# Kernel optimization log

Measured on AMD Instinct MI355X. Metric: run time of the kernel, lower is better.

Reference implementation:

```python
import jax, jax.numpy as jnp
import numpy as np

B, S, D, H, E, K = 4, 1024, 1024, 4096, 8, 2
CAPACITY_FACTOR = 2.0
T = B * S
CAP = int(T * CAPACITY_FACTOR * K / E)  # 2048


def setup_inputs() -> dict:
    key = jax.random.key(0)
    ks = jax.random.split(key, 6)
    std = 0.02
    return {
        "x": jax.random.normal(ks[0], (B, S, D), dtype=jnp.float32),
        "router_w": jax.random.normal(ks[1], (E, D), dtype=jnp.float32) * std,
        "w1": jax.random.normal(ks[2], (E, D, H), dtype=jnp.float32) * std,
        "b1": jnp.zeros((E, H), dtype=jnp.float32),
        "w2": jax.random.normal(ks[3], (E, H, D), dtype=jnp.float32) * std,
        "b2": jnp.zeros((E, D), dtype=jnp.float32),
    }


def reference(x, router_w, w1, b1, w2, b2):
    # Router (eval mode: no logit noise, no dropout)
    logits = jnp.einsum("bsd,ed->bse", x, router_w)            # [B,S,E]
    probs = jax.nn.softmax(logits, axis=-1)
    topk_p, topk_i = jax.lax.top_k(probs, K)                   # [B,S,K]
    gates = topk_p / jnp.sum(topk_p, axis=-1, keepdims=True)

    xt = x.reshape(T, D)                                        # tokens
    eidx = topk_i.reshape(T * K)                                # expert per slot
    g = gates.reshape(T * K)
    tok = jnp.arange(T * K) // K                                # token id per slot

    # position of each slot within its expert (first-come-first-served capacity)
    oh = jax.nn.one_hot(eidx, E, dtype=jnp.int32)               # [T*K, E]
    pos = jnp.sum((jnp.cumsum(oh, axis=0) - 1) * oh, axis=1)    # [T*K]
    keep = pos < CAP
    pos_c = jnp.where(keep, pos, CAP)                           # overflow -> padding row

    # dispatch: gather tokens into per-expert buffers [E, CAP, D]
    buf = jnp.zeros((E, CAP + 1, D), x.dtype).at[eidx, pos_c].set(xt[tok])
    inp = buf[:, :CAP]

    # per-expert FFN (exact-erf GELU matches torch nn.GELU default)
    h = jax.nn.gelu(jnp.einsum("ecd,edh->ech", inp, w1) + b1[:, None, :],
                    approximate=False)
    out_e = jnp.einsum("ech,eho->eco", h, w2) + b2[:, None, :]  # [E,CAP,D]

    # combine: gather back to slots, weight by gates, sum over k per token
    gathered = out_e[eidx, jnp.minimum(pos_c, CAP - 1)]         # [T*K, D]
    wslot = g * keep.astype(x.dtype)
    out = (gathered * wslot[:, None]).reshape(T, K, D).sum(axis=1).reshape(B, S, D)

    # load-balancing loss
    router_prob_per_expert = probs.mean(axis=(0, 1))            # [E]
    expert_usage = oh.sum(axis=0).astype(x.dtype) / (T * K)
    lb_loss = jnp.sum(router_prob_per_expert * expert_usage) * E
    return out, lb_loss
```

## Files before the change

kernel.cpp:

```cpp
#include <hip/hip_runtime.h>
#include <cstdint>
#include <cstddef>

#define TDIM 4096
#define DDIM 1024
#define HDIM 4096
#define EDIM 8
#define CAPD 2048
#define NSLOT 8192
#define NROUTERBLK 1024

typedef _Float16 f16;
typedef _Float16 f16x2 __attribute__((ext_vector_type(2)));
typedef _Float16 f16x4 __attribute__((ext_vector_type(4)));
typedef _Float16 f16x8 __attribute__((ext_vector_type(8)));
typedef float f32x4 __attribute__((ext_vector_type(4)));

__device__ __forceinline__ void gload16(const void* g, void* l) {
  __builtin_amdgcn_global_load_lds(
      (const __attribute__((address_space(1))) unsigned int*)g,
      (__attribute__((address_space(3))) unsigned int*)l, 16, 0, 0);
}

__device__ __forceinline__ float gelu_fast(float x) {
  float y = 1.5957691216057308f * (x + 0.044715f * x * x * x);
  y = fminf(y, 60.f);
  float e = __expf(y);
  return x * e * __builtin_amdgcn_rcpf(e + 1.f);
}

__global__ __launch_bounds__(256)
void transpose2_cvt(const float* __restrict__ w1, f16* __restrict__ w1t,
                    const float* __restrict__ w2, f16* __restrict__ w2t) {
  __shared__ float tile[128][65];
  const int z = blockIdx.z;
  const int id = blockIdx.y * 64 + blockIdx.x;
  const float* src; f16* dst; int R, C, rt, ct, e;
  if (z < EDIM) {
    e = z; src = w1; dst = w1t; R = DDIM; C = HDIM;
    ct = id & 63; rt = id >> 6;
  } else {
    e = z - EDIM; src = w2; dst = w2t; R = HDIM; C = DDIM;
    ct = id & 15; rt = id >> 4;
  }
  const int tid = threadIdx.x;
  const int r0 = rt * 128, c0 = ct * 64;
  const float* s = src + (size_t)e * R * C;
  f16* d = dst + (size_t)e * R * C;
  #pragma unroll
  for (int it = 0; it < 8; ++it) {
    const int idx = it * 256 + tid;
    const int row = idx >> 4, colq = (idx & 15) * 4;
    float4 v = *(const float4*)(s + (size_t)(r0 + row) * C + c0 + colq);
    tile[row][colq] = v.x; tile[row][colq + 1] = v.y;
    tile[row][colq + 2] = v.z; tile[row][colq + 3] = v.w;
  }
  __syncthreads();
  #pragma unroll
  for (int it = 0; it < 4; ++it) {
    const int idx = it * 256 + tid;
    const int c = idx >> 4, rw = (idx & 15) * 8;
    f16x8 o;
    #pragma unroll
    for (int j = 0; j < 8; ++j) o[j] = (f16)tile[rw + j][c];
    *(f16x8*)(d + (size_t)(c0 + c) * R + r0 + rw) = o;
  }
}

__global__ void router_k(const float* __restrict__ x, const float* __restrict__ rw,
                         int* __restrict__ eidx, float* __restrict__ gates,
                         float* __restrict__ bps) {
  __shared__ float lrw[EDIM * DDIM];
  __shared__ float wps[4][EDIM];
  const int tid = threadIdx.x, lane = tid & 63, wv = tid >> 6;
  for (int i = tid; i < EDIM * DDIM; i += 256) lrw[i] = rw[i];
  __syncthreads();
  const int t = blockIdx.x * 4 + wv;
  float acc[EDIM];
  #pragma unroll
  for (int e = 0; e < EDIM; ++e) acc[e] = 0.f;
  const float* xr = x + (size_t)t * DDIM;
  #pragma unroll
  for (int j = 0; j < DDIM / 64; ++j) {
    float xv = xr[j * 64 + lane];
    #pragma unroll
    for (int e = 0; e < EDIM; ++e) acc[e] += xv * lrw[e * DDIM + j * 64 + lane];
  }
  #pragma unroll
  for (int off = 32; off >= 1; off >>= 1) {
    #pragma unroll
    for (int e = 0; e < EDIM; ++e) acc[e] += __shfl_xor(acc[e], off);
  }
  float mx = acc[0];
  #pragma unroll
  for (int e = 1; e < EDIM; ++e) mx = fmaxf(mx, acc[e]);
  float p[EDIM], s = 0.f;
  #pragma unroll
  for (int e = 0; e < EDIM; ++e) { p[e] = expf(acc[e] - mx); s += p[e]; }
  float inv = 1.f / s;
  #pragma unroll
  for (int e = 0; e < EDIM; ++e) p[e] *= inv;
  int i1 = 0; float p1 = p[0];
  #pragma unroll
  for (int e = 1; e < EDIM; ++e) if (p[e] > p1) { p1 = p[e]; i1 = e; }
  int i2 = (i1 == 0) ? 1 : 0; float p2 = p[i2];
  #pragma unroll
  for (int e = 0; e < EDIM; ++e) if (e != i1 && p[e] > p2) { p2 = p[e]; i2 = e; }
  float gs = 1.f / (p1 + p2);
  if (lane == 0) {
    eidx[2 * t] = i1; eidx[2 * t + 1] = i2;
    gates[2 * t] = p1 * gs; gates[2 * t + 1] = p2 * gs;
    #pragma unroll
    for (int e = 0; e < EDIM; ++e) wps[wv][e] = p[e];
  }
  __syncthreads();
  if (tid < EDIM)
    bps[blockIdx.x * EDIM + tid] = wps[0][tid] + wps[1][tid] + wps[2][tid] + wps[3][tid];
}

__global__ void count_k(const int* __restrict__ eidx, int* __restrict__ cc) {
  __shared__ int h[EDIM];
  const int tid = threadIdx.x;
  if (tid < EDIM) h[tid] = 0;
  __syncthreads();
  atomicAdd(&h[eidx[blockIdx.x * 256 + tid]], 1);
  __syncthreads();
  if (tid < EDIM) cc[blockIdx.x * EDIM + tid] = h[tid];
}

__global__ void scan_k(const int* __restrict__ cc, const float* __restrict__ bps,
                       int* __restrict__ cb, int* __restrict__ counts,
                       int* __restrict__ rowsNeeded, float* __restrict__ lb_out) {
  __shared__ float red[32][EDIM];
  __shared__ int cnt_s[EDIM];
  const int tid = threadIdx.x;
  const int e = tid & 7, g = tid >> 3;
  float s = 0.f;
  for (int j = 0; j < 32; ++j) s += bps[(g + 32 * j) * EDIM + e];
  red[g][e] = s;
  __syncthreads();
  for (int st = 16; st >= 1; st >>= 1) {
    if (g < st) red[g][e] += red[g + st][e];
    __syncthreads();
  }
  if (tid < EDIM) {
    int base = 0;
    for (int c = 0; c < 32; ++c) { cb[c * EDIM + tid] = base; base += cc[c * EDIM + tid]; }
    counts[tid] = base;
    rowsNeeded[tid] = base < CAPD ? base : CAPD;
    cnt_s[tid] = base;
  }
  __syncthreads();
  if (tid == 0) {
    float lb = 0.f;
    for (int ee = 0; ee < EDIM; ++ee)
      lb += (red[0][ee] / (float)TDIM) * ((float)cnt_s[ee] / (float)NSLOT);
    lb_out[0] = lb * (float)EDIM;
  }
}

__global__ void pos_k(const int* __restrict__ eidx, const float* __restrict__ gates,
                      const int* __restrict__ cb, int* __restrict__ posa,
                      float* __restrict__ wslot) {
  __shared__ int wcnt[4][EDIM];
  const int tid = threadIdx.x, lane = tid & 63, wv = tid >> 6;
  const int slot = blockIdx.x * 256 + tid;
  const int e = eidx[slot];
  const unsigned long long below = (1ull << lane) - 1ull;
  int wavepos = 0;
  #pragma unroll
  for (int ee = 0; ee < EDIM; ++ee) {
    unsigned long long m = __ballot(e == ee);
    if (lane == 0) wcnt[wv][ee] = __popcll(m);
    if (e == ee) wavepos = __popcll(m & below);
  }
  __syncthreads();
  int off = 0;
  for (int w = 0; w < wv; ++w) off += wcnt[w][e];
  const int pos = cb[blockIdx.x * EDIM + e] + off + wavepos;
  posa[slot] = pos;
  wslot[slot] = (pos < CAPD) ? gates[slot] : 0.f;
}

__global__ void scatter2_k(const float* __restrict__ x, const int* __restrict__ eidx,
                           const int* __restrict__ posa, f16* __restrict__ buf) {
  const int t = blockIdx.x, lane = threadIdx.x;
  const int s0 = 2 * t, s1 = 2 * t + 1;
  const int p0 = posa[s0], p1 = posa[s1];
  const int e0 = eidx[s0], e1 = eidx[s1];
  const float4* src = (const float4*)(x + (size_t)t * DDIM);
  f16x4* d0 = (f16x4*)(buf + ((size_t)e0 * CAPD + p0) * DDIM);
  f16x4* d1 = (f16x4*)(buf + ((size_t)e1 * CAPD + p1) * DDIM);
  const bool w0 = p0 < CAPD, w1 = p1 < CAPD;
  #pragma unroll
  for (int j = 0; j < DDIM / 4 / 64; ++j) {
    float4 v = src[j * 64 + lane];
    f16x4 o; o.x = (f16)v.x; o.y = (f16)v.y; o.z = (f16)v.z; o.w = (f16)v.w;
    if (w0) d0[j * 64 + lane] = o;
    if (w1) d1[j * 64 + lane] = o;
  }
}

#define STAGE(hh, g) do { \
    const f16* s_ = sP[hh] + (g) * 64; \
    char* d_ = smem + (hh) * 8192 + wv * 1024; \
    gload16(s_, d_); \
    gload16(s_ + (size_t)32 * LD, d_ + 4096); \
  } while (0)

template<int KLEN, int LD, int N, int GELU, int NTH, int NKS, int NMT>
__global__ __launch_bounds__(256, 4)
void gemm128s(const f16* __restrict__ A, const f16* __restrict__ Bt,
              const float* __restrict__ bias, f16* __restrict__ C, size_t pstride,
              const int* __restrict__ rowsNeeded) {
  constexpr int NTT = KLEN / 64;
  __shared__ __align__(128) char smem[32768];
  const int wg = blockIdx.x;
  const int e = wg & 7;
  const int r = wg >> 3;
  const int ntl = r % NTH;
  const int ks = (r / NTH) % NKS;
  const int mt = (r / (NTH * NKS)) % NMT;
  const int nth = r / (NTH * NKS * NMT);
  const int nt = nth * NTH + ntl;
  if (mt * 128 >= rowsNeeded[e]) return;
  const int tid = threadIdx.x, lane = tid & 63, wv = tid >> 6;
  const int wr = wv >> 1, wc = wv & 1;
  const int ro = lane & 15, q4 = (lane >> 4) * 4;
  const int ko0b = (lane >> 4) * 16;
  const f16* aBase = A + ((size_t)e * CAPD + (size_t)mt * 128) * LD + (size_t)ks * KLEN;
  const f16* bBase = Bt + ((size_t)e * N + (size_t)nt * 128) * LD + (size_t)ks * KLEN;
  const int row0 = tid >> 3;
  const int sw0 = ((tid & 7) ^ (row0 & 7)) * 8;

  const f16* sP[4];
  sP[0] = aBase + (size_t)row0 * LD + sw0;
  sP[1] = sP[0] + (size_t)64 * LD;
  sP[2] = bBase + (size_t)row0 * LD + sw0;
  sP[3] = sP[2] + (size_t)64 * LD;

  int aoffs[4][2], boffs[4][2];
  #pragma unroll
  for (int m = 0; m < 4; ++m)
    #pragma unroll
    for (int k = 0; k < 2; ++k) {
      const int rh = wr * 64 + m * 16 + ro;
      aoffs[m][k] = rh * 128 + ((k * 64 + ko0b) ^ ((rh & 7) << 4));
      const int rb = wc * 64 + m * 16 + ro;
      boffs[m][k] = 16384 + rb * 128 + ((k * 64 + ko0b) ^ ((rb & 7) << 4));
    }

  f32x4 acc[4][4];
  #pragma unroll
  for (int m = 0; m < 4; ++m)
    #pragma unroll
    for (int n = 0; n < 4; ++n) acc[m][n] = (f32x4){0.f, 0.f, 0.f, 0.f};

  #pragma unroll 1
  for (int t = 0; t < NTT; ++t) {
    STAGE(0, t); STAGE(1, t); STAGE(2, t); STAGE(3, t);
    __syncthreads();
    f16x8 af[4][2], bf[4][2];
    #pragma unroll
    for (int m = 0; m < 4; ++m)
      #pragma unroll
      for (int k = 0; k < 2; ++k) {
        af[m][k] = *(const f16x8*)(smem + aoffs[m][k]);
        bf[m][k] = *(const f16x8*)(smem + boffs[m][k]);
      }
    #pragma unroll
    for (int k = 0; k < 2; ++k)
      #pragma unroll
      for (int m = 0; m < 4; ++m)
        #pragma unroll
        for (int n = 0; n < 4; ++n)
          acc[m][n] = __builtin_amdgcn_mfma_f32_16x16x32_f16(af[m][k], bf[n][k], acc[m][n], 0, 0, 0);
    __syncthreads();
  }

  float bv[4];
  #pragma unroll
  for (int n = 0; n < 4; ++n)
    bv[n] = (ks == 0) ? bias[e * N + nt * 128 + wc * 64 + n * 16 + ro] : 0.f;
  f16* Ct = (f16*)(smem + wv * 8192);
  #pragma unroll
  for (int m = 0; m < 4; ++m)
    #pragma unroll
    for (int n = 0; n < 4; ++n)
      #pragma unroll
      for (int i = 0; i < 4; ++i) {
        const int row = m * 16 + q4 + i;
        float v = acc[m][n][i] + bv[n];
        if (GELU) v = gelu_fast(v);
        *(f16*)((char*)Ct + row * 128 + (((n * 16 + ro) * 2) ^ (((row >> 2) & 3) << 5))) = (f16)v;
      }
  asm volatile("s_waitcnt lgkmcnt(0)" ::: "memory");
  __builtin_amdgcn_sched_barrier(0);
  f16* Cp = C + (size_t)ks * pstride;
  const size_t crow0 = (size_t)e * CAPD + mt * 128 + wr * 64;
  const int ccol0 = nt * 128 + wc * 64;
  #pragma unroll
  for (int j = 0; j < 8; ++j) {
    const int idx = j * 64 + lane;
    const int rr = idx >> 3, c2 = (idx & 7) * 16;
    f16x8 v = *(const f16x8*)((const char*)Ct + rr * 128 + (c2 ^ (((rr >> 2) & 3) << 5)));
    *(f16x8*)(Cp + (crow0 + rr) * N + ccol0 + (idx & 7) * 8) = v;
  }
}

__global__ void combine_k(const f16* __restrict__ pA, const f16* __restrict__ pB,
                          const int* __restrict__ eidx, const int* __restrict__ posa,
                          const float* __restrict__ wslot, float* __restrict__ out) {
  const int t = blockIdx.x, tid = threadIdx.x;
  const int s0 = 2 * t, s1 = 2 * t + 1;
  const int e0 = eidx[s0], e1 = eidx[s1];
  int p0 = posa[s0]; p0 = p0 < CAPD - 1 ? p0 : CAPD - 1;
  int p1 = posa[s1]; p1 = p1 < CAPD - 1 ? p1 : CAPD - 1;
  const float g0 = wslot[s0], g1 = wslot[s1];
  const size_t o0 = ((size_t)e0 * CAPD + p0) * DDIM;
  const size_t o1 = ((size_t)e1 * CAPD + p1) * DDIM;
  const f16x2* r0a = (const f16x2*)(pA + o0);
  const f16x2* r0b = (const f16x2*)(pB + o0);
  const f16x2* r1a = (const f16x2*)(pA + o1);
  const f16x2* r1b = (const f16x2*)(pB + o1);
  float2* o = (float2*)(out + (size_t)t * DDIM);
  #pragma unroll
  for (int j = tid; j < DDIM / 2; j += 256) {
    f16x2 a0 = r0a[j], a1 = r0b[j], b0 = r1a[j], b1 = r1b[j];
    o[j] = make_float2(
        g0 * ((float)a0.x + (float)a1.x) + g1 * ((float)b0.x + (float)b1.x),
        g0 * ((float)a0.y + (float)a1.y) + g1 * ((float)b0.y + (float)b1.y));
  }
}

extern "C" void kernel_launch(void* const* d_in, const int* in_sizes, int n_in,
                              void* d_out, int out_size, void* d_ws, size_t ws_size,
                              hipStream_t stream) {
  (void)in_sizes; (void)n_in; (void)out_size; (void)ws_size;
  const float* x  = (const float*)d_in[0];
  const float* rw = (const float*)d_in[1];
  const float* w1 = (const float*)d_in[2];
  const float* b1 = (const float*)d_in[3];
  const float* w2 = (const float*)d_in[4];
  const float* b2 = (const float*)d_in[5];
  float* out = (float*)d_out;

  char* ws = (char*)d_ws;
  size_t off = 0;
  auto alloc = [&](size_t b) { void* p = ws + off; off += (b + 255) & ~(size_t)255; return p; };
  f16* w1t   = (f16*)alloc((size_t)EDIM * DDIM * HDIM * 2);
  f16* w2t   = (f16*)alloc((size_t)EDIM * DDIM * HDIM * 2);
  f16* buf   = (f16*)alloc((size_t)EDIM * CAPD * DDIM * 2);
  f16* hbuf  = (f16*)alloc((size_t)EDIM * CAPD * HDIM * 2);
  const size_t PSTRIDE = (size_t)EDIM * CAPD * DDIM;
  f16* outeA = (f16*)alloc(PSTRIDE * 2);
  f16* outeB = (f16*)alloc(PSTRIDE * 2);
  int*   eidx   = (int*)alloc(NSLOT * 4);
  int*   posa   = (int*)alloc(NSLOT * 4);
  float* gatesA = (float*)alloc(NSLOT * 4);
  float* wslotA = (float*)alloc(NSLOT * 4);
  int*   cc     = (int*)alloc(32 * EDIM * 4);
  int*   cb     = (int*)alloc(32 * EDIM * 4);
  int*   counts = (int*)alloc(EDIM * 4);
  int*   rowsN  = (int*)alloc(EDIM * 4);
  float* bps    = (float*)alloc(NROUTERBLK * EDIM * 4);
  (void)outeB;

  transpose2_cvt<<<dim3(64, 8, 2 * EDIM), 256, 0, stream>>>(w1, w1t, w2, w2t);

  router_k<<<NROUTERBLK, 256, 0, stream>>>(x, rw, eidx, gatesA, bps);
  count_k<<<32, 256, 0, stream>>>(eidx, cc);
  scan_k<<<1, 256, 0, stream>>>(cc, bps, cb, counts, rowsN, out + (size_t)TDIM * DDIM);
  pos_k<<<32, 256, 0, stream>>>(eidx, gatesA, cb, posa, wslotA);
  scatter2_k<<<TDIM, 64, 0, stream>>>(x, eidx, posa, buf);

  gemm128s<DDIM, DDIM, HDIM, 1, 16, 1, 16><<<4096, 256, 0, stream>>>(
      buf, w1t, b1, hbuf, 0, rowsN);

  gemm128s<HDIM / 2, HDIM, DDIM, 0, 8, 2, 16><<<2048, 256, 0, stream>>>(
      hbuf, w2t, b2, outeA, PSTRIDE, rowsN);

  combine_k<<<TDIM, 256, 0, stream>>>(outeA, outeA + PSTRIDE, eidx, posa, wslotA, out);
}
```

Before: 293.7 us.

## Use async global-to-LDS loads with swizzled tiles in weight transpose; widen scatter stores

The weight transpose/convert kernel now uses 64x64 tiles loaded directly into LDS via global_load_lds with an XOR swizzle, replacing register-staged float4 loads into a padded 128x65 tile. It launches a flat 1D grid of smaller blocks with a higher occupancy hint, which reduces LDS use per block. Separately, the scatter kernel writes 16-byte f16x8 vectors instead of 8-byte f16x4. The aim is to cut load latency and bank conflicts in the transpose, which streams all expert weights every call, and to halve store instructions in the scatter. The swizzled indexing adds complexity and is a correctness risk.

```diff
diff --git a/kernel.cpp b/kernel.cpp
--- a/kernel.cpp
+++ b/kernel.cpp
@@ -29,41 +29,41 @@
   return x * e * __builtin_amdgcn_rcpf(e + 1.f);
 }
 
-__global__ __launch_bounds__(256)
+__global__ __launch_bounds__(256, 8)
 void transpose2_cvt(const float* __restrict__ w1, f16* __restrict__ w1t,
                     const float* __restrict__ w2, f16* __restrict__ w2t) {
-  __shared__ float tile[128][65];
-  const int z = blockIdx.z;
-  const int id = blockIdx.y * 64 + blockIdx.x;
-  const float* src; f16* dst; int R, C, rt, ct, e;
-  if (z < EDIM) {
-    e = z; src = w1; dst = w1t; R = DDIM; C = HDIM;
-    ct = id & 63; rt = id >> 6;
-  } else {
-    e = z - EDIM; src = w2; dst = w2t; R = HDIM; C = DDIM;
-    ct = id & 15; rt = id >> 4;
-  }
-  const int tid = threadIdx.x;
-  const int r0 = rt * 128, c0 = ct * 64;
-  const float* s = src + (size_t)e * R * C;
-  f16* d = dst + (size_t)e * R * C;
-  #pragma unroll
-  for (int it = 0; it < 8; ++it) {
+  __shared__ __align__(128) char smem[16384];
+  const int b = blockIdx.x;
+  const int half = b >> 13, within = b & 8191;
+  const int e = within >> 10, tile = within & 1023;
+  const float* src; f16* dst; int R, C, rt, ct;
+  if (half == 0) { src = w1; dst = w1t; R = DDIM; C = HDIM; ct = tile & 63; rt = tile >> 6; }
+  else           { src = w2; dst = w2t; R = HDIM; C = DDIM; ct = tile & 15; rt = tile >> 4; }
+  const int tid = threadIdx.x, wv = tid >> 6;
+  const int r0 = rt * 64, c0 = ct * 64;
+  const float* s = src + (size_t)e * R * C + (size_t)r0 * C + c0;
+  f16* d = dst + (size_t)e * R * C + (size_t)c0 * R + r0;
+  #pragma unroll
+  for (int i = 0; i < 4; ++i) {
+    const int chunk = i * 256 + tid;
+    const int row = chunk >> 4, s4 = chunk & 15;
+    const int sl = (s4 & 8) | ((s4 ^ (row >> 3)) & 7);
+    gload16(s + (size_t)row * C + sl * 4, smem + i * 4096 + wv * 1024);
+  }
+  __syncthreads();
+  #pragma unroll
+  for (int it = 0; it < 2; ++it) {
     const int idx = it * 256 + tid;
-    const int row = idx >> 4, colq = (idx & 15) * 4;
-    float4 v = *(const float4*)(s + (size_t)(r0 + row) * C + c0 + colq);
-    tile[row][colq] = v.x; tile[row][colq + 1] = v.y;
-    tile[row][colq + 2] = v.z; tile[row][colq + 3] = v.w;
-  }
-  __syncthreads();
-  #pragma unroll
-  for (int it = 0; it < 4; ++it) {
-    const int idx = it * 256 + tid;
-    const int c = idx >> 4, rw = (idx & 15) * 8;
+    const int c = idx >> 3, w = idx & 7;
+    const int slotc = ((c >> 2) & 8) | (((c >> 2) ^ w) & 7);
+    const int cb4 = (c & 3) * 4;
     f16x8 o;
     #pragma unroll
-    for (int j = 0; j < 8; ++j) o[j] = (f16)tile[rw + j][c];
-    *(f16x8*)(d + (size_t)(c0 + c) * R + r0 + rw) = o;
+    for (int j = 0; j < 8; ++j) {
+      const float v = *(const float*)(smem + (8 * w + j) * 256 + slotc * 16 + cb4);
+      o[j] = (f16)v;
+    }
+    *(f16x8*)(d + (size_t)c * R + 8 * w) = o;
   }
 }
 
@@ -189,13 +189,16 @@
   const int p0 = posa[s0], p1 = posa[s1];
   const int e0 = eidx[s0], e1 = eidx[s1];
   const float4* src = (const float4*)(x + (size_t)t * DDIM);
-  f16x4* d0 = (f16x4*)(buf + ((size_t)e0 * CAPD + p0) * DDIM);
-  f16x4* d1 = (f16x4*)(buf + ((size_t)e1 * CAPD + p1) * DDIM);
+  f16x8* d0 = (f16x8*)(buf + ((size_t)e0 * CAPD + p0) * DDIM);
+  f16x8* d1 = (f16x8*)(buf + ((size_t)e1 * CAPD + p1) * DDIM);
   const bool w0 = p0 < CAPD, w1 = p1 < CAPD;
   #pragma unroll
-  for (int j = 0; j < DDIM / 4 / 64; ++j) {
-    float4 v = src[j * 64 + lane];
-    f16x4 o; o.x = (f16)v.x; o.y = (f16)v.y; o.z = (f16)v.z; o.w = (f16)v.w;
+  for (int j = 0; j < 2; ++j) {
+    float4 a = src[j * 128 + lane * 2];
+    float4 b = src[j * 128 + lane * 2 + 1];
+    f16x8 o;
+    o[0] = (f16)a.x; o[1] = (f16)a.y; o[2] = (f16)a.z; o[3] = (f16)a.w;
+    o[4] = (f16)b.x; o[5] = (f16)b.y; o[6] = (f16)b.z; o[7] = (f16)b.w;
     if (w0) d0[j * 64 + lane] = o;
     if (w1) d1[j * 64 + lane] = o;
   }
@@ -366,7 +369,7 @@
   float* bps    = (float*)alloc(NROUTERBLK * EDIM * 4);
   (void)outeB;
 
-  transpose2_cvt<<<dim3(64, 8, 2 * EDIM), 256, 0, stream>>>(w1, w1t, w2, w2t);
+  transpose2_cvt<<<16384, 256, 0, stream>>>(w1, w1t, w2, w2t);
 
   router_k<<<NROUTERBLK, 256, 0, stream>>>(x, rw, eidx, gatesA, bps);
   count_k<<<32, 256, 0, stream>>>(eidx, cc);
```

New measurement: 293.7 us. Within noise of the previous version (+0.0%).
